# Kernel tuning notes

Hardware: AMD Instinct MI355X
Metric: run time of the kernel (lower is better)

The kernel has to match this reference:

```python
import jax, jax.numpy as jnp
import numpy as np

N, E, F, EF, T, C = 50000, 500000, 8, 4, 12, 32


def setup_inputs() -> dict:
    key = jax.random.key(0)
    ks = jax.random.split(key, 16)
    g = lambda i, shape, s=0.2: jax.random.normal(ks[i], shape, jnp.float32) * s
    return {
        "x": jax.random.normal(ks[0], (N, F, T), jnp.float32),
        "edge_index": jax.random.randint(ks[1], (2, E), 0, N),
        "edge_features": jax.random.normal(ks[2], (E, EF), jnp.float32),
        # feature_linear (F -> F)
        "feat_W": g(3, (F, F)), "feat_b": jnp.zeros((F,), jnp.float32),
        # edge_features_linear (EF -> 1)
        "ef_W": g(4, (EF, 1)), "ef_b": jnp.zeros((1,), jnp.float32),
        # A3TGCN attention over periods
        "attention": jax.random.uniform(ks[5], (T,), jnp.float32),
        # TGCN GCNConv weights (F -> C), bias included (PyG default)
        "conv_z_W": g(6, (F, C)), "conv_z_b": jnp.zeros((C,), jnp.float32),
        "conv_r_W": g(7, (F, C)), "conv_r_b": jnp.zeros((C,), jnp.float32),
        "conv_h_W": g(8, (F, C)), "conv_h_b": jnp.zeros((C,), jnp.float32),
        # TGCN gate linears (2C -> C)
        "lin_z_W": g(9, (2 * C, C)), "lin_z_b": jnp.zeros((C,), jnp.float32),
        "lin_r_W": g(10, (2 * C, C)), "lin_r_b": jnp.zeros((C,), jnp.float32),
        "lin_h_W": g(11, (2 * C, C)), "lin_h_b": jnp.zeros((C,), jnp.float32),
        # output head (C -> T)
        "head_W": g(12, (C, T)), "head_b": jnp.zeros((T,), jnp.float32),
    }


def _gcn_norm(edge_index, edge_weight, num_nodes):
    """PyG gcn_norm with add_self_loops=True (fill 1), flow source_to_target."""
    loops = jnp.arange(num_nodes)
    row = jnp.concatenate([edge_index[0], loops])  # sources
    col = jnp.concatenate([edge_index[1], loops])  # targets
    w = jnp.concatenate([edge_weight, jnp.ones((num_nodes,), edge_weight.dtype)])
    deg = jax.ops.segment_sum(w, col, num_segments=num_nodes)
    dinv = jnp.where(deg > 0, jax.lax.rsqrt(jnp.maximum(deg, 1e-12)), 0.0)
    norm = dinv[row] * w * dinv[col]
    return row, col, norm


def _forward(x, edge_index, edge_features, feat_W, feat_b, ef_W, ef_b,
             attention, conv_z_W, conv_z_b, conv_r_W, conv_r_b, conv_h_W,
             conv_h_b, lin_z_W, lin_z_b, lin_r_W, lin_r_b, lin_h_W, lin_h_b,
             head_W, head_b):
    num_nodes = x.shape[0]
    # feature linear over F: [N,F,T] -> [T,N,F]
    xt = jnp.transpose(x, (2, 0, 1)) @ feat_W + feat_b  # [T,N,F]
    # edge weight MLP: [E,EF] -> [E], relu
    ew = jax.nn.relu((edge_features @ ef_W + ef_b)[:, 0])
    row, col, norm = _gcn_norm(edge_index, ew, num_nodes)

    def gcn(h, W, b):
        msg = (h @ W)[row] * norm[:, None]  # [E+N, C]
        return jax.ops.segment_sum(msg, col, num_segments=num_nodes) + b

    def tgcn_cell(x_t):
        # A3TGCN passes H=None each period -> H starts at zeros every period
        H = jnp.zeros((num_nodes, C), x_t.dtype)
        Z = jax.nn.sigmoid(
            jnp.concatenate([gcn(x_t, conv_z_W, conv_z_b), H], 1) @ lin_z_W + lin_z_b)
        R = jax.nn.sigmoid(
            jnp.concatenate([gcn(x_t, conv_r_W, conv_r_b), H], 1) @ lin_r_W + lin_r_b)
        H_tilde = jnp.tanh(
            jnp.concatenate([gcn(x_t, conv_h_W, conv_h_b), H * R], 1) @ lin_h_W + lin_h_b)
        return Z * H + (1.0 - Z) * H_tilde

    probs = jax.nn.softmax(attention)

    def step(acc, inputs):
        x_t, p = inputs
        return acc + p * tgcn_cell(x_t), None

    H_accum, _ = jax.lax.scan(step, jnp.zeros((num_nodes, C), x.dtype), (xt, probs))
    h = jax.nn.relu(H_accum)
    return h @ head_W + head_b  # [N, T]


def reference(x, edge_index, edge_features, feat_W, feat_b, ef_W, ef_b,
              attention, conv_z_W, conv_z_b, conv_r_W, conv_r_b, conv_h_W,
              conv_h_b, lin_z_W, lin_z_b, lin_r_W, lin_r_b, lin_h_W, lin_h_b,
              head_W, head_b):
    return _forward(x, edge_index, edge_features, feat_W, feat_b, ef_W, ef_b,
                    attention, conv_z_W, conv_z_b, conv_r_W, conv_r_b,
                    conv_h_W, conv_h_b, lin_z_W, lin_z_b, lin_r_W, lin_r_b,
                    lin_h_W, lin_h_b, head_W, head_b)
```

## Files before the change

kernel.cpp:

```cpp
#include <hip/hip_runtime.h>
#include <math.h>

#define NN 50000
#define NE 500000
#define FD 8
#define EFD 4
#define TD 12
#define CD 32
#define FT (FD*TD)
#define SLOTS 48
#define ZB 49
#define ZV4 25000
#define PB 98
#define L2E 1.4426950408889634f
#define MASK56 ((1ULL << 56) - 1)
#define K56 (1.0f / 4294967296.0f)

typedef float f32x2 __attribute__((ext_vector_type(2)));

__global__ __launch_bounds__(512) void kInit(
    float4* __restrict__ zp, int4* __restrict__ ep4,
    const float* __restrict__ feat_W, const float* __restrict__ feat_b,
    const float* __restrict__ attention,
    const float* __restrict__ conv_z_W, const float* __restrict__ conv_z_b,
    const float* __restrict__ conv_h_W, const float* __restrict__ conv_h_b,
    const float* __restrict__ lin_z_W, const float* __restrict__ lin_z_b,
    const float* __restrict__ lin_h_W, const float* __restrict__ lin_h_b,
    float* __restrict__ consts)
{
    int tid = threadIdx.x;
    if (blockIdx.x < ZB) {
        int i = blockIdx.x * 512 + tid;
        if (i < ZV4) zp[i] = make_float4(0.f, 0.f, 0.f, 0.f);
        return;
    }
    if (blockIdx.x < ZB + PB) {
        int n = (blockIdx.x - ZB) * 512 + tid;
        if (n < NN) {
            int4 pad = make_int4(n, 0, n, 0);
            int4* p = ep4 + n * (SLOTS/2);
            p[0] = pad; p[1] = pad; p[2] = pad; p[3] = pad;
        }
        return;
    }
    __shared__ float WL[2][FD*CD];
    int half = tid >> 8;
    int idx  = tid & 255;
    int f = idx >> 5, c = idx & 31;
    float scale = half ? 2.f * L2E : L2E;
    const float* convW = half ? conv_h_W : conv_z_W;
    const float* linW  = half ? lin_h_W  : lin_z_W;
    float acc = 0.f;
    #pragma unroll
    for (int k = 0; k < CD; ++k)
        acc += convW[f*CD + k] * linW[k*CD + c];
    WL[half][idx] = acc;
    __syncthreads();
    float m = 0.f;
    #pragma unroll
    for (int g = 0; g < FD; ++g)
        m += feat_W[f*FD + g] * WL[half][g*CD + c];
    consts[half*256 + idx] = m * scale;
    if (f == 0) {
        float a = 0.f;
        #pragma unroll
        for (int g = 0; g < FD; ++g)
            a += feat_b[g] * WL[half][g*CD + c];
        consts[512 + half*32 + c] = a * scale;
        const float* convB = half ? conv_h_b : conv_z_b;
        const float* linB  = half ? lin_h_b : lin_z_b;
        float cc = linB[c];
        #pragma unroll
        for (int k = 0; k < CD; ++k)
            cc += convB[k] * linW[k*CD + c];
        consts[576 + half*32 + c] = cc * scale;
    }
    if (tid == 0) {
        float mx = attention[0];
        for (int t = 1; t < TD; ++t) mx = fmaxf(mx, attention[t]);
        float e[TD], sum = 0.f;
        for (int t = 0; t < TD; ++t) { e[t] = expf(attention[t] - mx); sum += e[t]; }
        for (int t = 0; t < TD; ++t) consts[640 + t] = e[t] / sum;
    }
}

__global__ void kB1(const int* __restrict__ ei, const float* __restrict__ ef,
                    const float* __restrict__ ef_W, const float* __restrict__ ef_b,
                    unsigned long long* __restrict__ dc, int2* __restrict__ ep)
{
    int e = blockIdx.x * blockDim.x + threadIdx.x;
    if (e >= NE) return;
    float4 f4 = ((const float4*)ef)[e];
    float w = ef_b[0] + f4.x*ef_W[0] + f4.y*ef_W[1] + f4.z*ef_W[2] + f4.w*ef_W[3];
    if (w <= 0.f) return;
    int r = ei[e], c = ei[NE + e];
    unsigned long long pack = (1ULL << 56)
        | (unsigned long long)(w * 4294967296.0f);
    unsigned long long old = atomicAdd(&dc[c], pack);
    int pos = (int)(old >> 56);
    if (pos < SLOTS) ep[c * SLOTS + pos] = make_int2(r, __float_as_int(w));
}

__global__ __launch_bounds__(256) void kGE(
    const float* __restrict__ x, const unsigned long long* __restrict__ dc,
    const int2* __restrict__ ep, const float* __restrict__ consts,
    const float* __restrict__ head_W, const float* __restrict__ head_b,
    float* __restrict__ out)
{
    __shared__ float headW[CD*TD];
    __shared__ float ylds[8*FT];
    __shared__ float hlds[8*33];
    int tid = threadIdx.x;
    int c0 = tid & 31;
    int gg = tid >> 5;
    float mzr[FD], mhr[FD];
    #pragma unroll
    for (int f = 0; f < FD; ++f) {
        mzr[f] = consts[f*CD + c0];
        mhr[f] = consts[256 + f*CD + c0];
    }
    float azc = consts[512 + c0], ahc = consts[544 + c0];
    float czc = consts[576 + c0], chc = consts[608 + c0];
    float pt[TD];
    #pragma unroll
    for (int t = 0; t < TD; ++t) pt[t] = consts[640 + t];
    headW[tid] = head_W[tid];
    if (tid < CD*TD - 256) headW[256 + tid] = head_W[256 + tid];
    int base = blockIdx.x * 8;
    int n = base + gg;

    unsigned long long vn = dc[n];
    float di = rsqrtf((float)(vn & MASK56) * K56 + 1.0f);
    float d2 = di * di;
    int m = (int)(vn >> 56);
    if (m > SLOTS) m = SLOTS;
    const float* xrow = x + (size_t)n * FT + c0 * 3;
    float3 xs = *(const float3*)xrow;
    float acc0 = d2*xs.x, acc1 = d2*xs.y, acc2 = d2*xs.z;
    int st = n * SLOTS;
    int2 q = ep[st + (c0 & 7)];
    unsigned long long sd = dc[q.x];
    float ds = rsqrtf((float)(sd & MASK56) * K56 + 1.0f);
    float vvl = __int_as_float(q.y) * ds * di;
    float sv = d2;
    #pragma unroll
    for (int i = 0; i < 8; ++i) {
        int   si = __shfl(q.x, i, 32);
        float vi = __shfl(vvl, i, 32);
        float3 xr = *(const float3*)(x + (size_t)si * FT + c0 * 3);
        acc0 += vi*xr.x; acc1 += vi*xr.y; acc2 += vi*xr.z;
        sv += vi;
    }
    for (int j = st + 8, en = st + m; j < en; ++j) {
        int2 p0 = ep[j];
        unsigned long long td = dc[p0.x];
        float tds = rsqrtf((float)(td & MASK56) * K56 + 1.0f);
        float v0 = __int_as_float(p0.y) * tds * di;
        float3 xr = *(const float3*)(x + (size_t)p0.x * FT + c0 * 3);
        acc0 += v0*xr.x; acc1 += v0*xr.y; acc2 += v0*xr.z;
        sv += v0;
    }
    float* yw = ylds + gg * FT + c0 * 3;
    yw[0] = acc0; yw[1] = acc1; yw[2] = acc2;
    float sn = sv;
    __syncthreads();

    const float4* yf4 = (const float4*)(ylds + gg * FT);
    float bz = czc + sn * azc;
    float bh = chc + sn * ahc;
    f32x2 pz2[6], ph2[6];
    #pragma unroll
    for (int k = 0; k < 6; ++k) {
        pz2[k].x = bz; pz2[k].y = bz;
        ph2[k].x = bh; ph2[k].y = bh;
    }
    #pragma unroll
    for (int f = 0; f < FD; ++f) {
        float4 ya = yf4[f*3 + 0], yb = yf4[f*3 + 1], yc = yf4[f*3 + 2];
        f32x2 y2[6];
        y2[0].x = ya.x; y2[0].y = ya.y;  y2[1].x = ya.z; y2[1].y = ya.w;
        y2[2].x = yb.x; y2[2].y = yb.y;  y2[3].x = yb.z; y2[3].y = yb.w;
        y2[4].x = yc.x; y2[4].y = yc.y;  y2[5].x = yc.z; y2[5].y = yc.w;
        f32x2 mz2, mh2;
        mz2.x = mzr[f]; mz2.y = mzr[f];
        mh2.x = mhr[f]; mh2.y = mhr[f];
        #pragma unroll
        for (int k = 0; k < 6; ++k) {
            asm volatile("v_pk_fma_f32 %0, %1, %2, %0"
                         : "+v"(pz2[k]) : "v"(y2[k]), "v"(mz2));
            asm volatile("v_pk_fma_f32 %0, %1, %2, %0"
                         : "+v"(ph2[k]) : "v"(y2[k]), "v"(mh2));
        }
    }
    float acc = 0.f;
    #pragma unroll
    for (int k = 0; k < 6; ++k) {
        #pragma unroll
        for (int h = 0; h < 2; ++h) {
            float pzv = (h == 0) ? pz2[k].x : pz2[k].y;
            float phv = (h == 0) ? ph2[k].x : ph2[k].y;
            float ez, eh;
            asm("v_exp_f32 %0, %1" : "=v"(ez) : "v"(pzv));
            asm("v_exp_f32 %0, %1" : "=v"(eh) : "v"(phv));
            float omz = __builtin_amdgcn_rcpf(1.f + ez);
            float th  = 1.f - 2.f * __builtin_amdgcn_rcpf(1.f + eh);
            acc += pt[2*k + h] * omz * th;
        }
    }
    hlds[gg*33 + c0] = fmaxf(acc, 0.f);
    __syncthreads();

    if (tid < 8*TD) {
        int n0 = tid / TD, tt = tid - n0*TD;
        float v = head_b[tt];
        const float* hn = hlds + n0*33;
        #pragma unroll
        for (int cc = 0; cc < CD; ++cc) v += hn[cc] * headW[cc*TD + tt];
        out[(size_t)(base + n0)*TD + tt] = v;
    }
}

extern "C" void kernel_launch(void* const* d_in, const int* in_sizes, int n_in,
                              void* d_out, int out_size, void* d_ws, size_t ws_size,
                              hipStream_t stream)
{
    const float* x      = (const float*)d_in[0];
    const int*   ei     = (const int*)  d_in[1];
    const float* ef     = (const float*)d_in[2];
    const float* feat_W = (const float*)d_in[3];
    const float* feat_b = (const float*)d_in[4];
    const float* ef_W   = (const float*)d_in[5];
    const float* ef_b   = (const float*)d_in[6];
    const float* att    = (const float*)d_in[7];
    const float* czW    = (const float*)d_in[8];
    const float* czb    = (const float*)d_in[9];
    const float* chW    = (const float*)d_in[12];
    const float* chb    = (const float*)d_in[13];
    const float* lzW    = (const float*)d_in[14];
    const float* lzb    = (const float*)d_in[15];
    const float* lhW    = (const float*)d_in[18];
    const float* lhb    = (const float*)d_in[19];
    const float* hW     = (const float*)d_in[20];
    const float* hb     = (const float*)d_in[21];
    float* out = (float*)d_out;

    unsigned long long* dc  = (unsigned long long*)d_ws;
    float*              cst = (float*)(dc + NN);
    int2*               ep  = (int2*)(cst + 1024);

    kInit<<<ZB + PB + 1, 512, 0, stream>>>((float4*)dc, (int4*)ep,
                                           feat_W, feat_b, att, czW, czb,
                                           chW, chb, lzW, lzb, lhW, lhb, cst);
    kB1<<<(NE + 255)/256, 256, 0, stream>>>(ei, ef, ef_W, ef_b, dc, ep);
    kGE<<<NN/8, 256, 0, stream>>>(x, dc, ep, cst, hW, hb, out);
}
```

Measured before the change: 57.51 us.

## Drop edge-slot padding init and shrink gather blocks to two nodes

The init kernel no longer pre-fills the first eight edge slots per node with self-index padding. The gather kernel now guards the first-eight-slot load with slot < m and substitutes a zero weight, which removes 98 blocks of padding writes. Separately, kGE blocks shrink from 8 nodes (256 threads) to 2 nodes (64 threads), giving finer scheduling granularity at the cost of reloading the head weights into shared memory in four times as many blocks.

```diff
diff --git a/kernel.cpp b/kernel.cpp
--- a/kernel.cpp
+++ b/kernel.cpp
@@ -11,7 +11,6 @@
 #define SLOTS 48
 #define ZB 49
 #define ZV4 25000
-#define PB 98
 #define L2E 1.4426950408889634f
 #define MASK56 ((1ULL << 56) - 1)
 #define K56 (1.0f / 4294967296.0f)
@@ -19,7 +18,7 @@
 typedef float f32x2 __attribute__((ext_vector_type(2)));
 
 __global__ __launch_bounds__(512) void kInit(
-    float4* __restrict__ zp, int4* __restrict__ ep4,
+    float4* __restrict__ zp,
     const float* __restrict__ feat_W, const float* __restrict__ feat_b,
     const float* __restrict__ attention,
     const float* __restrict__ conv_z_W, const float* __restrict__ conv_z_b,
@@ -32,15 +31,6 @@
     if (blockIdx.x < ZB) {
         int i = blockIdx.x * 512 + tid;
         if (i < ZV4) zp[i] = make_float4(0.f, 0.f, 0.f, 0.f);
-        return;
-    }
-    if (blockIdx.x < ZB + PB) {
-        int n = (blockIdx.x - ZB) * 512 + tid;
-        if (n < NN) {
-            int4 pad = make_int4(n, 0, n, 0);
-            int4* p = ep4 + n * (SLOTS/2);
-            p[0] = pad; p[1] = pad; p[2] = pad; p[3] = pad;
-        }
         return;
     }
     __shared__ float WL[2][FD*CD];
@@ -101,15 +91,15 @@
     if (pos < SLOTS) ep[c * SLOTS + pos] = make_int2(r, __float_as_int(w));
 }
 
-__global__ __launch_bounds__(256) void kGE(
+__global__ __launch_bounds__(64) void kGE(
     const float* __restrict__ x, const unsigned long long* __restrict__ dc,
     const int2* __restrict__ ep, const float* __restrict__ consts,
     const float* __restrict__ head_W, const float* __restrict__ head_b,
     float* __restrict__ out)
 {
     __shared__ float headW[CD*TD];
-    __shared__ float ylds[8*FT];
-    __shared__ float hlds[8*33];
+    __shared__ float ylds[2*FT];
+    __shared__ float hlds[2*33];
     int tid = threadIdx.x;
     int c0 = tid & 31;
     int gg = tid >> 5;
@@ -124,10 +114,9 @@
     float pt[TD];
     #pragma unroll
     for (int t = 0; t < TD; ++t) pt[t] = consts[640 + t];
-    headW[tid] = head_W[tid];
-    if (tid < CD*TD - 256) headW[256 + tid] = head_W[256 + tid];
-    int base = blockIdx.x * 8;
-    int n = base + gg;
+    #pragma unroll
+    for (int k = 0; k < 6; ++k) headW[tid + 64*k] = head_W[tid + 64*k];
+    int n = blockIdx.x * 2 + gg;
 
     unsigned long long vn = dc[n];
     float di = rsqrtf((float)(vn & MASK56) * K56 + 1.0f);
@@ -138,10 +127,15 @@
     float3 xs = *(const float3*)xrow;
     float acc0 = d2*xs.x, acc1 = d2*xs.y, acc2 = d2*xs.z;
     int st = n * SLOTS;
-    int2 q = ep[st + (c0 & 7)];
-    unsigned long long sd = dc[q.x];
-    float ds = rsqrtf((float)(sd & MASK56) * K56 + 1.0f);
-    float vvl = __int_as_float(q.y) * ds * di;
+    int slot = c0 & 7;
+    int2 q = make_int2(n, 0);
+    float vvl = 0.f;
+    if (slot < m) {
+        q = ep[st + slot];
+        unsigned long long sd = dc[q.x];
+        float ds = rsqrtf((float)(sd & MASK56) * K56 + 1.0f);
+        vvl = __int_as_float(q.y) * ds * di;
+    }
     float sv = d2;
     #pragma unroll
     for (int i = 0; i < 8; ++i) {
@@ -210,13 +204,13 @@
     hlds[gg*33 + c0] = fmaxf(acc, 0.f);
     __syncthreads();
 
-    if (tid < 8*TD) {
+    if (tid < 2*TD) {
         int n0 = tid / TD, tt = tid - n0*TD;
         float v = head_b[tt];
         const float* hn = hlds + n0*33;
         #pragma unroll
         for (int cc = 0; cc < CD; ++cc) v += hn[cc] * headW[cc*TD + tt];
-        out[(size_t)(base + n0)*TD + tt] = v;
+        out[(size_t)(blockIdx.x*2 + n0)*TD + tt] = v;
     }
 }
 
@@ -248,9 +242,8 @@
     float*              cst = (float*)(dc + NN);
     int2*               ep  = (int2*)(cst + 1024);
 
-    kInit<<<ZB + PB + 1, 512, 0, stream>>>((float4*)dc, (int4*)ep,
-                                           feat_W, feat_b, att, czW, czb,
-                                           chW, chb, lzW, lzb, lhW, lhb, cst);
+    kInit<<<ZB + 1, 512, 0, stream>>>((float4*)dc, feat_W, feat_b, att,
+                                      czW, czb, chW, chb, lzW, lzb, lhW, lhb, cst);
     kB1<<<(NE + 255)/256, 256, 0, stream>>>(ei, ef, ef_W, ef_b, dc, ep);
-    kGE<<<NN/8, 256, 0, stream>>>(x, dc, ep, cst, hW, hb, out);
-}
+    kGE<<<NN/2, 64, 0, stream>>>(x, dc, ep, cst, hW, hb, out);
+}
```

Measured after the change: 56.35 us, median of 2. -2.0%, faster.
